# Kernel tuning notes

Measured on AMD Instinct MI355X. Metric: run time of the kernel, lower is better.

The kernel has to match this reference:

```python
import jax, jax.numpy as jnp
import numpy as np

B, V, T = 256, 128000, 16
TOP_K = 100          # min(100, V - n_targets) == 100 since V >> T
TARGET_MARGIN = 1.0
EPS = 1e-8
NEG = -1e30          # sentinel so masked target slots never enter top-k


def setup_inputs() -> dict:
    key = jax.random.key(0)
    k1, k2 = jax.random.split(key)
    # Non-negative sparse activations (SPLADE-style relu output) in [0,1)
    sparse_rep = jax.random.uniform(k1, (B, V), dtype=jnp.float32)
    # Fixed-length padded target id lists (all rows valid -> n_valid = B)
    target_ids = jax.random.randint(k2, (B, T), 0, V).astype(jnp.int64)
    return {"sparse_rep": sparse_rep, "target_ids": target_ids}


def reference(sparse_rep, target_ids):
    # [B, T] gather of target activations (one batched gather, no per-row loop)
    tgt = jnp.take_along_axis(sparse_rep, target_ids, axis=1)
    # -log(a + eps), per-row mean then batch mean == global mean (fixed T)
    target_loss = -jnp.mean(jnp.log(tgt + EPS))
    # hinge margin on target activations
    margin_loss = jnp.mean(jax.nn.relu(TARGET_MARGIN - tgt))
    # mask out target columns per row, then top-k over remaining vocab
    rows = jnp.arange(sparse_rep.shape[0])[:, None]          # [B, 1]
    masked = sparse_rep.at[rows, target_ids].set(NEG)        # [B, V]
    top_vals = jax.lax.top_k(masked, TOP_K)[0]               # [B, TOP_K]
    negative_loss = jnp.mean(top_vals)
    return (target_loss, margin_loss, negative_loss)
```

## Files before the change

kernel.cpp:

```cpp
#include <hip/hip_runtime.h>
#include <cstddef>
#include <cstdint>

#define B_      256
#define V_      128000
#define T_      16
#define TOPK_   100
#define NF4     (V_ / 4)
#define NHIST   4096
#define SLICES  5
#define F4S     (NF4 / SLICES)
#define ITERS   (F4S / 256)
#define UNROLL  5
#define CAP_BLK 256
#define CAP_ROW 2048
#define T0      0.998f


__global__ void zero_kernel(float* o, int* ws_cnt, int* ws_of) {
    int t = threadIdx.x;
    if (t < 3) o[t] = 0.f;
    if (t < B_) { ws_cnt[t] = 0; ws_of[t] = 0; }
}

__global__ __launch_bounds__(256) void collect_kernel(
        const float* __restrict__ sparse,
        const int*   __restrict__ tids,
        float*       __restrict__ ws_cand,
        int*         __restrict__ ws_cnt,
        int*         __restrict__ ws_of) {
    __shared__ int   s_ids[T_];
    __shared__ float s_buf[CAP_BLK];
    __shared__ int   s_n;
    __shared__ int   s_gbase;

    const int blk = blockIdx.x;
    const int row = blk / SLICES;
    const int sl  = blk - row * SLICES;
    const int tid = threadIdx.x;

    if (tid < T_) s_ids[tid] = tids[row * T_ + tid];
    if (tid == 0) s_n = 0;
    __syncthreads();

    const float4* __restrict__ rp4 = (const float4*)(sparse + (size_t)row * V_);
    const int base = sl * F4S + tid;

    for (int it = 0; it < ITERS; it += UNROLL) {
        float4 v[UNROLL];
        #pragma unroll
        for (int u = 0; u < UNROLL; ++u)
            v[u] = rp4[base + (it + u) * 256];
        #pragma unroll
        for (int u = 0; u < UNROLL; ++u) {
            const int col = (base + (it + u) * 256) << 2;
            float xs[4] = {v[u].x, v[u].y, v[u].z, v[u].w};
            #pragma unroll
            for (int c = 0; c < 4; ++c) {
                float x = xs[c];
                if (x >= T0) {
                    int cc = col + c;
                    bool is_t = false;
                    #pragma unroll
                    for (int j = 0; j < T_; ++j) is_t |= (cc == s_ids[j]);
                    if (!is_t) {
                        int k = atomicAdd(&s_n, 1);
                        if (k < CAP_BLK) s_buf[k] = x;
                    }
                }
            }
        }
    }
    __syncthreads();

    int n = min(s_n, CAP_BLK);
    if (tid == 0) {
        s_gbase = atomicAdd(ws_cnt + row, n);
        if (s_n > CAP_BLK) atomicExch(ws_of + row, 1);
    }
    __syncthreads();
    int gbase = s_gbase;
    float* __restrict__ cand = ws_cand + (size_t)row * CAP_ROW;
    for (int i = tid; i < n; i += 256) cand[gbase + i] = s_buf[i];
}

__global__ __launch_bounds__(256) void reduce_kernel(
        const float* __restrict__ sparse,
        const int*   __restrict__ tids,
        const float* __restrict__ ws_cand,
        const int*   __restrict__ ws_cnt,
        const int*   __restrict__ ws_of,
        float*       __restrict__ out) {
    __shared__ float    s_cand[CAP_ROW];
    __shared__ unsigned s_hist[NHIST];
    __shared__ int      s_ids[T_];
    __shared__ int      s_cnt;
    __shared__ int      s_bstar;
    __shared__ float    s_red[4];

    const int row = blockIdx.x;
    const int tid = threadIdx.x;
    const float* __restrict__ rp = sparse + (size_t)row * V_;

    if (tid < T_) s_ids[tid] = tids[row * T_ + tid];
    __syncthreads();

    if (tid < T_) {
        float x  = rp[s_ids[tid]];
        float tl = -logf(x + 1e-8f);
        float ml = fmaxf(1.0f - x, 0.0f);
        #pragma unroll
        for (int off = 8; off > 0; off >>= 1) {
            tl += __shfl_down(tl, off);
            ml += __shfl_down(ml, off);
        }
        if (tid == 0) {
            atomicAdd(out + 0, tl * (1.0f / (B_ * T_)));
            atomicAdd(out + 1, ml * (1.0f / (B_ * T_)));
        }
    }

    int cnt = ws_cnt[row];
    bool bad = (cnt < TOPK_) || (cnt > CAP_ROW) || (ws_of[row] != 0);

    if (!bad) {
        const float* cand = ws_cand + (size_t)row * CAP_ROW;
        for (int i = tid; i < cnt; i += 256) s_cand[i] = cand[i];
        __syncthreads();
    } else {
        for (int i = tid; i < NHIST; i += 256) s_hist[i] = 0u;
        if (tid == 0) s_cnt = 0;
        __syncthreads();
        const float4* rp4 = (const float4*)rp;
        for (int i = tid; i < NF4; i += 256) {
            float4 v = rp4[i];
            float xs[4] = {v.x, v.y, v.z, v.w};
            #pragma unroll
            for (int c = 0; c < 4; ++c) {
                int b = (int)(xs[c] * (float)NHIST);
                b = min(max(b, 0), NHIST - 1);
                atomicAdd(&s_hist[b], 1u);
            }
        }
        __syncthreads();
        if (tid == 0) {
            for (int j = 0; j < T_; ++j) {
                int id = s_ids[j];
                bool dup = false;
                for (int q = 0; q < j; ++q) dup = dup || (s_ids[q] == id);
                if (!dup) {
                    int b = (int)(rp[id] * (float)NHIST);
                    b = min(max(b, 0), NHIST - 1);
                    s_hist[b]--;
                }
            }
            int acc = 0, b = NHIST - 1;
            for (; b >= 0; --b) {
                acc += (int)s_hist[b];
                if (acc >= TOPK_) break;
            }
            s_bstar = max(b, 0);
        }
        __syncthreads();
        int bstar = s_bstar;
        for (int i = tid; i < NF4; i += 256) {
            float4 v = rp4[i];
            int col = i << 2;
            float xs[4] = {v.x, v.y, v.z, v.w};
            #pragma unroll
            for (int c = 0; c < 4; ++c) {
                float x = xs[c];
                int b = (int)(x * (float)NHIST);
                b = min(max(b, 0), NHIST - 1);
                if (b >= bstar) {
                    int cc = col + c;
                    bool is_t = false;
                    #pragma unroll
                    for (int j = 0; j < T_; ++j) is_t |= (cc == s_ids[j]);
                    if (!is_t) {
                        int k = atomicAdd(&s_cnt, 1);
                        if (k < CAP_ROW) s_cand[k] = x;
                    }
                }
            }
        }
        __syncthreads();
        cnt = min(s_cnt, CAP_ROW);
    }

    float sum = 0.f;
    for (int i = tid; i < cnt; i += 256) {
        float x = s_cand[i];
        int rank = 0;
        for (int j = 0; j < cnt; ++j) {
            float y = s_cand[j];
            rank += (y > x) ? 1 : ((y == x && j < i) ? 1 : 0);
        }
        if (rank < TOPK_) sum += x;
    }

    #pragma unroll
    for (int off = 32; off > 0; off >>= 1) sum += __shfl_down(sum, off);
    if ((tid & 63) == 0) s_red[tid >> 6] = sum;
    __syncthreads();
    if (tid == 0) {
        float tot = s_red[0] + s_red[1] + s_red[2] + s_red[3];
        atomicAdd(out + 2, tot * (1.0f / (B_ * TOPK_)));
    }
}

extern "C" void kernel_launch(void* const* d_in, const int* in_sizes, int n_in,
                              void* d_out, int out_size, void* d_ws, size_t ws_size,
                              hipStream_t stream) {
    const float* sparse = (const float*)d_in[0];
    const int*   tids   = (const int*)d_in[1];
    float*       out    = (float*)d_out;
    int*         ws_cnt  = (int*)d_ws;
    int*         ws_of   = (int*)((char*)d_ws + 1024);
    float*       ws_cand = (float*)((char*)d_ws + 4096);

    zero_kernel<<<1, 256, 0, stream>>>(out, ws_cnt, ws_of);
    collect_kernel<<<B_ * SLICES, 256, 0, stream>>>(sparse, tids, ws_cand, ws_cnt, ws_of);
    reduce_kernel<<<B_, 256, 0, stream>>>(sparse, tids, ws_cand, ws_cnt, ws_of, out);
}
```

Before: 218.6 us.

## Fuse collect and reduce kernels using last-block-done per row

```diff
diff --git a/kernel.cpp b/kernel.cpp
--- a/kernel.cpp
+++ b/kernel.cpp
@@ -17,22 +17,29 @@
 #define T0      0.998f
 
 
-__global__ void zero_kernel(float* o, int* ws_cnt, int* ws_of) {
+__global__ void zero_kernel(float* o, int* ws_cnt, int* ws_of, int* ws_done) {
     int t = threadIdx.x;
     if (t < 3) o[t] = 0.f;
-    if (t < B_) { ws_cnt[t] = 0; ws_of[t] = 0; }
+    if (t < B_) { ws_cnt[t] = 0; ws_of[t] = 0; ws_done[t] = 0; }
 }
 
-__global__ __launch_bounds__(256) void collect_kernel(
+__global__ __launch_bounds__(256) void fused_kernel(
         const float* __restrict__ sparse,
         const int*   __restrict__ tids,
         float*       __restrict__ ws_cand,
         int*         __restrict__ ws_cnt,
-        int*         __restrict__ ws_of) {
+        int*         __restrict__ ws_of,
+        int*         __restrict__ ws_done,
+        float*       __restrict__ out) {
     __shared__ int   s_ids[T_];
     __shared__ float s_buf[CAP_BLK];
     __shared__ int   s_n;
     __shared__ int   s_gbase;
+    __shared__ int   s_last;
+    __shared__ float s_cand[NHIST];
+    __shared__ int   s_cnt;
+    __shared__ int   s_bstar;
+    __shared__ float s_red[4];
 
     const int blk = blockIdx.x;
     const int row = blk / SLICES;
@@ -43,7 +50,8 @@
     if (tid == 0) s_n = 0;
     __syncthreads();
 
-    const float4* __restrict__ rp4 = (const float4*)(sparse + (size_t)row * V_);
+    const float* __restrict__ rp = sparse + (size_t)row * V_;
+    const float4* __restrict__ rp4 = (const float4*)rp;
     const int base = sl * F4S + tid;
 
     for (int it = 0; it < ITERS; it += UNROLL) {
@@ -79,31 +87,21 @@
         if (s_n > CAP_BLK) atomicExch(ws_of + row, 1);
     }
     __syncthreads();
-    int gbase = s_gbase;
-    float* __restrict__ cand = ws_cand + (size_t)row * CAP_ROW;
-    for (int i = tid; i < n; i += 256) cand[gbase + i] = s_buf[i];
-}
-
-__global__ __launch_bounds__(256) void reduce_kernel(
-        const float* __restrict__ sparse,
-        const int*   __restrict__ tids,
-        const float* __restrict__ ws_cand,
-        const int*   __restrict__ ws_cnt,
-        const int*   __restrict__ ws_of,
-        float*       __restrict__ out) {
-    __shared__ float    s_cand[CAP_ROW];
-    __shared__ unsigned s_hist[NHIST];
-    __shared__ int      s_ids[T_];
-    __shared__ int      s_cnt;
-    __shared__ int      s_bstar;
-    __shared__ float    s_red[4];
-
-    const int row = blockIdx.x;
-    const int tid = threadIdx.x;
-    const float* __restrict__ rp = sparse + (size_t)row * V_;
-
-    if (tid < T_) s_ids[tid] = tids[row * T_ + tid];
-    __syncthreads();
+    {
+        int gbase = s_gbase;
+        float* __restrict__ cand = ws_cand + (size_t)row * CAP_ROW;
+        for (int i = tid; i < n; i += 256) cand[gbase + i] = s_buf[i];
+    }
+
+    __threadfence();
+    if (tid == 0) {
+        int prev = atomicAdd(ws_done + row, 1);
+        s_last = (prev == SLICES - 1) ? 1 : 0;
+    }
+    __syncthreads();
+    if (!s_last) return;
+    __threadfence();
+
 
     if (tid < T_) {
         float x  = rp[s_ids[tid]];
@@ -120,18 +118,19 @@
         }
     }
 
-    int cnt = ws_cnt[row];
-    bool bad = (cnt < TOPK_) || (cnt > CAP_ROW) || (ws_of[row] != 0);
+    int cnt = atomicAdd(ws_cnt + row, 0);
+    int of  = atomicAdd(ws_of + row, 0);
+    bool bad = (cnt < TOPK_) || (cnt > CAP_ROW) || (of != 0);
 
     if (!bad) {
         const float* cand = ws_cand + (size_t)row * CAP_ROW;
         for (int i = tid; i < cnt; i += 256) s_cand[i] = cand[i];
         __syncthreads();
     } else {
+        unsigned* s_hist = (unsigned*)s_cand;
         for (int i = tid; i < NHIST; i += 256) s_hist[i] = 0u;
         if (tid == 0) s_cnt = 0;
         __syncthreads();
-        const float4* rp4 = (const float4*)rp;
         for (int i = tid; i < NF4; i += 256) {
             float4 v = rp4[i];
             float xs[4] = {v.x, v.y, v.z, v.w};
@@ -217,9 +216,10 @@
     float*       out    = (float*)d_out;
     int*         ws_cnt  = (int*)d_ws;
     int*         ws_of   = (int*)((char*)d_ws + 1024);
+    int*         ws_done = (int*)((char*)d_ws + 2048);
     float*       ws_cand = (float*)((char*)d_ws + 4096);
 
-    zero_kernel<<<1, 256, 0, stream>>>(out, ws_cnt, ws_of);
-    collect_kernel<<<B_ * SLICES, 256, 0, stream>>>(sparse, tids, ws_cand, ws_cnt, ws_of);
-    reduce_kernel<<<B_, 256, 0, stream>>>(sparse, tids, ws_cand, ws_cnt, ws_of, out);
+    zero_kernel<<<1, 256, 0, stream>>>(out, ws_cnt, ws_of, ws_done);
+    fused_kernel<<<B_ * SLICES, 256, 0, stream>>>(sparse, tids, ws_cand,
+                                                  ws_cnt, ws_of, ws_done, out);
 }
```

Measured after the change: 413.3 us. 1.89x slower.
